# Optimization experiments

Measured on AMD Instinct MI355X. Metric: run time of the kernel, lower is better.

Reference implementation:

```python
import jax, jax.numpy as jnp
import numpy as np

IN_C = 256
OUT_C = 256
KQ_C = 256
HEADS = 8

def setup_inputs() -> dict:
    key = jax.random.key(0)
    kx, kq, kk, kv = jax.random.split(key, 4)
    N, T = 4, 2048
    x = jax.random.normal(kx, (N, IN_C, T), dtype=jnp.float32)
    # Conv1d(kernel_size=1, bias=False) weights: [out, in]
    s = 1.0 / np.sqrt(IN_C)
    Wq = jax.random.uniform(kq, (KQ_C, IN_C), dtype=jnp.float32, minval=-s, maxval=s)
    Wk = jax.random.uniform(kk, (KQ_C, IN_C), dtype=jnp.float32, minval=-s, maxval=s)
    Wv = jax.random.uniform(kv, (OUT_C, IN_C), dtype=jnp.float32, minval=-s, maxval=s)
    return {"x": x, "Wq": Wq, "Wk": Wk, "Wv": Wv}

def reference(x, Wq, Wk, Wv):
    N, C, T = x.shape
    H = HEADS
    dk = KQ_C // H   # head dim for q/k
    dv = OUT_C // H  # head dim for v
    # 1x1 conv == channel matmul: [N,C,T] -> [N,out,T]
    q = jnp.einsum('oc,nct->not', Wq, x).reshape(N, H, dk, T)
    k = jnp.einsum('oc,nct->not', Wk, x).reshape(N, H, dk, T)
    v = jnp.einsum('oc,nct->not', Wv, x).reshape(N, H, dv, T)
    # scores: [N,H,T,T] = q^T k, scaled
    scores = jnp.einsum('nhdt,nhds->nhts', q, k) / np.sqrt(dk).astype(jnp.float32)
    attn = jax.nn.softmax(scores, axis=-1)
    # out: [N,H,T,dv] -> [N,H,dv,T] -> [N,OUT_C,T]
    out = jnp.einsum('nhts,nhds->nhdt', attn, v)
    return out.reshape(N, OUT_C, T)
```

## Files before the change

kernel.cpp:

```cpp
#include <hip/hip_runtime.h>


typedef float f32x4 __attribute__((ext_vector_type(4)));
typedef short short8 __attribute__((ext_vector_type(8)));
typedef short short4v __attribute__((ext_vector_type(4)));

#define WS_Q 0u
#define WS_K (4u << 20)
#define WS_V (8u << 20)
#define WS_X (12u << 20)
#define WS_W (16u << 20)
#define WS_OP (20u << 20)

__device__ __forceinline__ unsigned short f2bf(float f) {
  unsigned int u = __builtin_bit_cast(unsigned int, f);
  u += 0x7FFFu + ((u >> 16) & 1u);
  return (unsigned short)(u >> 16);
}

__device__ __forceinline__ int pack_bf16rn(float a, float b) {
  unsigned int ua = __builtin_bit_cast(unsigned int, a) + 0x8000u;
  unsigned int ub = __builtin_bit_cast(unsigned int, b) + 0x8000u;
  return __builtin_amdgcn_perm(ub, ua, 0x07060302);
}

__global__ __launch_bounds__(256) void pack_kernel(
    const float* __restrict__ x, const float* __restrict__ Wq,
    const float* __restrict__ Wk, const float* __restrict__ Wv,
    unsigned short* __restrict__ ws) {
  const int tid = threadIdx.x;
  const int lane = tid & 63;
  const int wv = tid >> 6;
  const int lc = lane & 15, lq = lane >> 4;
  const int b = blockIdx.x;
  alignas(16) unsigned short tmp[8];
  if (b < 1024) {
    const int r = b * 4 + wv;
    const int kc = r & 7, tt = (r >> 3) & 127, n = r >> 10;
    const int t = tt * 16 + lc;
    const int c0 = kc * 32 + lq * 8;
    const float* src = x + (size_t)(n * 256 + c0) * 2048 + t;
#pragma unroll
    for (int j = 0; j < 8; ++j) tmp[j] = f2bf(src[(size_t)j * 2048]);
    unsigned short* dst = ws + (WS_X >> 1) + (size_t)r * 512 + lane * 8;
    *(int4*)dst = *(const int4*)tmp;
  } else {
    const int r = (b - 1024) * 4 + wv;
    const int kc = r & 7, ot = (r >> 3) & 15, wi = r >> 7;
    const float* W = (wi == 0) ? Wq : (wi == 1) ? Wk : Wv;
    const float scale = (wi == 0) ? 0.25503492f : 1.0f;
    const int o = ot * 16 + lc;
    const int c0 = kc * 32 + lq * 8;
    const float* src = W + o * 256 + c0;
#pragma unroll
    for (int j = 0; j < 8; ++j) tmp[j] = f2bf(src[j] * scale);
    unsigned short* dst = ws + (WS_W >> 1) + (size_t)r * 512 + lane * 8;
    *(int4*)dst = *(const int4*)tmp;
  }
}

__global__ __launch_bounds__(256) void proj_kernel(unsigned short* __restrict__ ws) {
  __shared__ unsigned short eps[4][2048];
  const int tid = threadIdx.x, lane = tid & 63, w = tid >> 6;
  const int lc = lane & 15, lq = lane >> 4;
  const int tt2 = blockIdx.x;
  const int n = blockIdx.y;
  const int wi = blockIdx.z;
  const unsigned short* Xb = ws + (WS_X >> 1);
  const unsigned short* Wb = ws + (WS_W >> 1);

  short8 af[2][8];
#pragma unroll
  for (int mt = 0; mt < 2; ++mt)
#pragma unroll
    for (int kc = 0; kc < 8; ++kc)
      af[mt][kc] = *(const short8*)(Xb + ((size_t)((n * 128 + tt2 * 2 + mt) * 8 + kc) * 512 + lane * 8));

  f32x4 acc[2][4];
#pragma unroll
  for (int mt = 0; mt < 2; ++mt)
#pragma unroll
    for (int nt = 0; nt < 4; ++nt) {
      f32x4 z = {0.f, 0.f, 0.f, 0.f};
      acc[mt][nt] = z;
    }

#pragma unroll
  for (int kc = 0; kc < 8; ++kc) {
    short8 bf[4];
#pragma unroll
    for (int nt = 0; nt < 4; ++nt)
      bf[nt] = *(const short8*)(Wb + ((size_t)((wi * 16 + w * 4 + nt) * 8 + kc) * 512 + lane * 8));
#pragma unroll
    for (int mt = 0; mt < 2; ++mt)
#pragma unroll
      for (int nt = 0; nt < 4; ++nt)
        acc[mt][nt] = __builtin_amdgcn_mfma_f32_16x16x32_bf16(af[mt][kc], bf[nt], acc[mt][nt], 0, 0, 0);
  }

  if (wi < 2) {
    unsigned short* ep = eps[w];
#pragma unroll
    for (int mt = 0; mt < 2; ++mt)
#pragma unroll
      for (int nt = 0; nt < 4; ++nt) {
        const int m2 = ((nt & 1) << 1) | (lc >> 3);
        const int base = ((mt * 2 + (nt >> 1)) << 9) + (m2 << 7) + (lq << 5) + (lc & 7);
#pragma unroll
        for (int r = 0; r < 4; ++r)
          ep[base + ((r ^ m2) << 3)] = f2bf(acc[mt][nt][r]);
      }
    const int swzl = lane ^ (lane >> 4);
    unsigned short* dst = ws + ((wi == 0) ? (WS_Q >> 1) : (WS_K >> 1));
#pragma unroll
    for (int rl = 0; rl < 4; ++rl) {
      int4 v = *(const int4*)(ep + (rl << 9) + swzl * 8);
      const int mt = rl >> 1, hh = rl & 1;
      const int nh = n * 8 + w * 2 + hh;
      const int ttg = tt2 * 2 + mt;
      *(int4*)(dst + ((size_t)(nh * 128 + ttg) * 64 + lane) * 8) = v;
    }
  } else {
    const int kb = tt2 >> 1, sbp = tt2 & 1;
#pragma unroll
    for (int nt = 0; nt < 4; ++nt) {
      const int nh = n * 8 + w * 2 + (nt >> 1);
      const int dt = nt & 1;
      alignas(16) unsigned short tmp[8];
#pragma unroll
      for (int mt = 0; mt < 2; ++mt)
#pragma unroll
        for (int r = 0; r < 4; ++r) tmp[mt * 4 + r] = f2bf(acc[mt][nt][r]);
      unsigned short* dstv = ws + (WS_V >> 1) +
          ((size_t)((((nh * 32 + kb) * 2 + dt) * 2 + sbp)) * 64 + lane) * 8;
      *(int4*)dstv = *(const int4*)tmp;
    }
  }
}

template <int KS>
__global__ __launch_bounds__(128, 5) void attn_kernel(
    const unsigned short* __restrict__ ws, float* __restrict__ out,
    unsigned short* __restrict__ opart, float* __restrict__ lpart) {
  const int tid = threadIdx.x;
  const int lane = tid & 63, wv = tid >> 6;
  const int lc = lane & 15, quad = lane >> 4;
  constexpr int CH = 32 * KS;
  const int c = blockIdx.x & (CH - 1);
  const int qx = blockIdx.x / CH;
  const int nh = c & 31;
  const int ks = c >> 5;
  const int qw = qx * 2 + wv;
  constexpr int NKB = 32 / KS;
  const int kb0 = ks * NKB;

  const unsigned short* Qw = ws + (WS_Q >> 1) + ((size_t)(nh * 128 + qw * 2)) * 512;
  const unsigned short* Kb = ws + (WS_K >> 1) + (size_t)nh * 65536;
  const unsigned short* Vb = ws + (WS_V >> 1) + (size_t)nh * 65536;

  short8 qf[2];
  qf[0] = *(const short8*)(Qw + lane * 8);
  qf[1] = *(const short8*)(Qw + 512 + lane * 8);

  f32x4 acc[2][2];
#pragma unroll
  for (int mt = 0; mt < 2; ++mt)
#pragma unroll
    for (int dt = 0; dt < 2; ++dt) {
      f32x4 z = {0.f, 0.f, 0.f, 0.f};
      acc[mt][dt] = z;
    }
  float lsum[2] = {0.f, 0.f};

  for (int kb = kb0; kb < kb0 + NKB; ++kb) {
    const unsigned short* kp = Kb + (size_t)kb * 2048 + lane * 8;
    const unsigned short* vp = Vb + (size_t)kb * 2048 + lane * 8;
    short8 kf[4], vvr[4];
#pragma unroll
    for (int sb = 0; sb < 4; ++sb) kf[sb] = *(const short8*)(kp + sb * 512);
#pragma unroll
    for (int u = 0; u < 4; ++u) vvr[u] = *(const short8*)(vp + u * 512);

    short4v pf[2][4];
#pragma unroll
    for (int mt = 0; mt < 2; ++mt) {
      f32x4 st[4];
#pragma unroll
      for (int sb = 0; sb < 4; ++sb) {
        f32x4 z = {0.f, 0.f, 0.f, 0.f};
        st[sb] = __builtin_amdgcn_mfma_f32_16x16x32_bf16(kf[sb], qf[mt], z, 0, 0, 0);
      }
#pragma unroll
      for (int sb = 0; sb < 4; ++sb) {
        float p0 = __builtin_amdgcn_exp2f(st[sb][0]);
        float p1 = __builtin_amdgcn_exp2f(st[sb][1]);
        float p2 = __builtin_amdgcn_exp2f(st[sb][2]);
        float p3 = __builtin_amdgcn_exp2f(st[sb][3]);
        lsum[mt] += (p0 + p1) + (p2 + p3);
        int2 pi;
        pi.x = pack_bf16rn(p0, p1);
        pi.y = pack_bf16rn(p2, p3);
        pf[mt][sb] = __builtin_bit_cast(short4v, pi);
      }
    }

    short4v vf[4][2];
#pragma unroll
    for (int dt = 0; dt < 2; ++dt)
#pragma unroll
      for (int sbp = 0; sbp < 2; ++sbp) {
        short8 t = vvr[dt * 2 + sbp];
        vf[sbp * 2 + 0][dt] = __builtin_shufflevector(t, t, 0, 1, 2, 3);
        vf[sbp * 2 + 1][dt] = __builtin_shufflevector(t, t, 4, 5, 6, 7);
      }
#pragma unroll
    for (int sb = 0; sb < 4; ++sb)
#pragma unroll
      for (int mt = 0; mt < 2; ++mt) {
        acc[mt][0] = __builtin_amdgcn_mfma_f32_16x16x16bf16_1k(pf[mt][sb], vf[sb][0], acc[mt][0], 0, 0, 0);
        acc[mt][1] = __builtin_amdgcn_mfma_f32_16x16x16bf16_1k(pf[mt][sb], vf[sb][1], acc[mt][1], 0, 0, 0);
      }
  }

#pragma unroll
  for (int mt = 0; mt < 2; ++mt) {
    lsum[mt] += __shfl_xor(lsum[mt], 16);
    lsum[mt] += __shfl_xor(lsum[mt], 32);
  }

  if constexpr (KS == 1) {
    const int chbase = (nh >> 3) * 256 + (nh & 7) * 32;
#pragma unroll
    for (int mt = 0; mt < 2; ++mt) {
      float is[4];
#pragma unroll
      for (int r = 0; r < 4; ++r) is[r] = 1.0f / __shfl(lsum[mt], quad * 4 + r);
      const int tb = qw * 32 + mt * 16 + quad * 4;
#pragma unroll
      for (int dt = 0; dt < 2; ++dt) {
        f32x4 ov;
#pragma unroll
        for (int r = 0; r < 4; ++r) ov[r] = acc[mt][dt][r] * is[r];
        *(f32x4*)(out + (size_t)(chbase + dt * 16 + lc) * 2048 + tb) = ov;
      }
    }
  } else {
    const size_t ob = (size_t)(ks * 32 + nh) * 32 * 2048;
#pragma unroll
    for (int mt = 0; mt < 2; ++mt) {
      const int tb = qw * 32 + mt * 16 + quad * 4;
#pragma unroll
      for (int dt = 0; dt < 2; ++dt) {
        int2 pi;
        pi.x = pack_bf16rn(acc[mt][dt][0], acc[mt][dt][1]);
        pi.y = pack_bf16rn(acc[mt][dt][2], acc[mt][dt][3]);
        *(int2*)(opart + ob + (size_t)(dt * 16 + lc) * 2048 + tb) = pi;
      }
      if (quad == 0)
        lpart[(size_t)(ks * 32 + nh) * 2048 + qw * 32 + mt * 16 + lc] = lsum[mt];
    }
  }
}

template <int KS>
__global__ __launch_bounds__(256) void finalize_kernel(
    const unsigned short* __restrict__ opart, const float* __restrict__ lpart,
    float* __restrict__ out) {
  const int f = blockIdx.x * 256 + threadIdx.x;
  const int t4 = f & 511;
  const int c = f >> 9;
  const int n = c >> 8, ch = c & 255;
  const int nh = n * 8 + (ch >> 5), d = ch & 31;
  float o[4] = {0.f, 0.f, 0.f, 0.f};
  float l[4] = {0.f, 0.f, 0.f, 0.f};
#pragma unroll
  for (int ks = 0; ks < KS; ++ks) {
    const short4v ov = *(const short4v*)(opart + ((size_t)(ks * 32 + nh) * 32 + d) * 2048 + t4 * 4);
    const float4 lv = *(const float4*)(lpart + (size_t)(ks * 32 + nh) * 2048 + t4 * 4);
#pragma unroll
    for (int i = 0; i < 4; ++i) {
      const unsigned int u = ((unsigned int)(unsigned short)ov[i]) << 16;
      o[i] += __builtin_bit_cast(float, u);
    }
    l[0] += lv.x; l[1] += lv.y; l[2] += lv.z; l[3] += lv.w;
  }
  float4 r;
  r.x = o[0] / l[0]; r.y = o[1] / l[1]; r.z = o[2] / l[2]; r.w = o[3] / l[3];
  *(float4*)(out + (size_t)f * 4) = r;
}

extern "C" void kernel_launch(void* const* d_in, const int* in_sizes, int n_in,
                              void* d_out, int out_size, void* d_ws, size_t ws_size,
                              hipStream_t stream) {
  const float* x = (const float*)d_in[0];
  const float* Wq = (const float*)d_in[1];
  const float* Wk = (const float*)d_in[2];
  const float* Wv = (const float*)d_in[3];
  unsigned short* ws = (unsigned short*)d_ws;
  float* out = (float*)d_out;
  (void)in_sizes; (void)n_in; (void)out_size;

  pack_kernel<<<1120, 256, 0, stream>>>(x, Wq, Wk, Wv, ws);
  proj_kernel<<<dim3(64, 4, 3), 256, 0, stream>>>(ws);

  char* wsb = (char*)d_ws;
  unsigned short* opart = (unsigned short*)(wsb + WS_OP);
  if (ws_size >= ((size_t)41u << 20)) {
    float* lpart = (float*)(wsb + WS_OP + ((size_t)4 * 4u << 20));
    attn_kernel<4><<<4096, 128, 0, stream>>>(ws, out, opart, lpart);
    finalize_kernel<4><<<2048, 256, 0, stream>>>(opart, lpart, out);
  } else if (ws_size >= ((size_t)30u << 20)) {
    float* lpart = (float*)(wsb + WS_OP + ((size_t)2 * 4u << 20));
    attn_kernel<2><<<2048, 128, 0, stream>>>(ws, out, opart, lpart);
    finalize_kernel<2><<<2048, 256, 0, stream>>>(opart, lpart, out);
  } else {
    attn_kernel<1><<<1024, 128, 0, stream>>>(ws, out, nullptr, nullptr);
  }
}
```

Measured before the change: 111.7 us.

## Double per-wave query tile to 64 rows to reuse K/V loads

Each wave now processes four 16-row query tiles instead of two, so every K and V fragment loaded from global memory is reused across twice as many queries. This halves the grid size and the total K/V traffic. The loop is reordered so QK MFMAs, exp and PV MFMAs are interleaved per key sub-block. The cost is higher register pressure, which is why the occupancy hint drops from 5 to 4 blocks per CU, and there are fewer blocks to fill the machine.

```diff
diff --git a/kernel.cpp b/kernel.cpp
--- a/kernel.cpp
+++ b/kernel.cpp
@@ -139,14 +139,14 @@
 }
 
 template <int KS>
-__global__ __launch_bounds__(128, 5) void attn_kernel(
+__global__ __launch_bounds__(128, 4) void attn_kernel(
     const unsigned short* __restrict__ ws, float* __restrict__ out,
     unsigned short* __restrict__ opart, float* __restrict__ lpart) {
   const int tid = threadIdx.x;
   const int lane = tid & 63, wv = tid >> 6;
   const int lc = lane & 15, quad = lane >> 4;
   constexpr int CH = 32 * KS;
-  const int c = blockIdx.x & (CH - 1);
+  const int c = blockIdx.x % CH;
   const int qx = blockIdx.x / CH;
   const int nh = c & 31;
   const int ks = c >> 5;
@@ -154,23 +154,23 @@
   constexpr int NKB = 32 / KS;
   const int kb0 = ks * NKB;
 
-  const unsigned short* Qw = ws + (WS_Q >> 1) + ((size_t)(nh * 128 + qw * 2)) * 512;
+  const unsigned short* Qw = ws + (WS_Q >> 1) + ((size_t)(nh * 128 + qw * 4)) * 512;
   const unsigned short* Kb = ws + (WS_K >> 1) + (size_t)nh * 65536;
   const unsigned short* Vb = ws + (WS_V >> 1) + (size_t)nh * 65536;
 
-  short8 qf[2];
-  qf[0] = *(const short8*)(Qw + lane * 8);
-  qf[1] = *(const short8*)(Qw + 512 + lane * 8);
-
-  f32x4 acc[2][2];
-#pragma unroll
-  for (int mt = 0; mt < 2; ++mt)
+  short8 qf[4];
+#pragma unroll
+  for (int mt = 0; mt < 4; ++mt) qf[mt] = *(const short8*)(Qw + mt * 512 + lane * 8);
+
+  f32x4 acc[4][2];
+#pragma unroll
+  for (int mt = 0; mt < 4; ++mt)
 #pragma unroll
     for (int dt = 0; dt < 2; ++dt) {
       f32x4 z = {0.f, 0.f, 0.f, 0.f};
       acc[mt][dt] = z;
     }
-  float lsum[2] = {0.f, 0.f};
+  float lsum[4] = {0.f, 0.f, 0.f, 0.f};
 
   for (int kb = kb0; kb < kb0 + NKB; ++kb) {
     const unsigned short* kp = Kb + (size_t)kb * 2048 + lane * 8;
@@ -181,49 +181,42 @@
 #pragma unroll
     for (int u = 0; u < 4; ++u) vvr[u] = *(const short8*)(vp + u * 512);
 
-    short4v pf[2][4];
-#pragma unroll
-    for (int mt = 0; mt < 2; ++mt) {
+#pragma unroll
+    for (int sb = 0; sb < 4; ++sb) {
       f32x4 st[4];
 #pragma unroll
-      for (int sb = 0; sb < 4; ++sb) {
+      for (int mt = 0; mt < 4; ++mt) {
         f32x4 z = {0.f, 0.f, 0.f, 0.f};
-        st[sb] = __builtin_amdgcn_mfma_f32_16x16x32_bf16(kf[sb], qf[mt], z, 0, 0, 0);
-      }
-#pragma unroll
-      for (int sb = 0; sb < 4; ++sb) {
-        float p0 = __builtin_amdgcn_exp2f(st[sb][0]);
-        float p1 = __builtin_amdgcn_exp2f(st[sb][1]);
-        float p2 = __builtin_amdgcn_exp2f(st[sb][2]);
-        float p3 = __builtin_amdgcn_exp2f(st[sb][3]);
+        st[mt] = __builtin_amdgcn_mfma_f32_16x16x32_bf16(kf[sb], qf[mt], z, 0, 0, 0);
+      }
+      short4v pfv[4];
+#pragma unroll
+      for (int mt = 0; mt < 4; ++mt) {
+        float p0 = __builtin_amdgcn_exp2f(st[mt][0]);
+        float p1 = __builtin_amdgcn_exp2f(st[mt][1]);
+        float p2 = __builtin_amdgcn_exp2f(st[mt][2]);
+        float p3 = __builtin_amdgcn_exp2f(st[mt][3]);
         lsum[mt] += (p0 + p1) + (p2 + p3);
         int2 pi;
         pi.x = pack_bf16rn(p0, p1);
         pi.y = pack_bf16rn(p2, p3);
-        pf[mt][sb] = __builtin_bit_cast(short4v, pi);
-      }
-    }
-
-    short4v vf[4][2];
-#pragma unroll
-    for (int dt = 0; dt < 2; ++dt)
-#pragma unroll
-      for (int sbp = 0; sbp < 2; ++sbp) {
-        short8 t = vvr[dt * 2 + sbp];
-        vf[sbp * 2 + 0][dt] = __builtin_shufflevector(t, t, 0, 1, 2, 3);
-        vf[sbp * 2 + 1][dt] = __builtin_shufflevector(t, t, 4, 5, 6, 7);
-      }
-#pragma unroll
-    for (int sb = 0; sb < 4; ++sb)
-#pragma unroll
-      for (int mt = 0; mt < 2; ++mt) {
-        acc[mt][0] = __builtin_amdgcn_mfma_f32_16x16x16bf16_1k(pf[mt][sb], vf[sb][0], acc[mt][0], 0, 0, 0);
-        acc[mt][1] = __builtin_amdgcn_mfma_f32_16x16x16bf16_1k(pf[mt][sb], vf[sb][1], acc[mt][1], 0, 0, 0);
-      }
-  }
-
-#pragma unroll
-  for (int mt = 0; mt < 2; ++mt) {
+        pfv[mt] = __builtin_bit_cast(short4v, pi);
+      }
+      const int sbp = sb >> 1, h = sb & 1;
+      short4v vf0 = h ? __builtin_shufflevector(vvr[sbp], vvr[sbp], 4, 5, 6, 7)
+                      : __builtin_shufflevector(vvr[sbp], vvr[sbp], 0, 1, 2, 3);
+      short4v vf1 = h ? __builtin_shufflevector(vvr[2 + sbp], vvr[2 + sbp], 4, 5, 6, 7)
+                      : __builtin_shufflevector(vvr[2 + sbp], vvr[2 + sbp], 0, 1, 2, 3);
+#pragma unroll
+      for (int mt = 0; mt < 4; ++mt) {
+        acc[mt][0] = __builtin_amdgcn_mfma_f32_16x16x16bf16_1k(pfv[mt], vf0, acc[mt][0], 0, 0, 0);
+        acc[mt][1] = __builtin_amdgcn_mfma_f32_16x16x16bf16_1k(pfv[mt], vf1, acc[mt][1], 0, 0, 0);
+      }
+    }
+  }
+
+#pragma unroll
+  for (int mt = 0; mt < 4; ++mt) {
     lsum[mt] += __shfl_xor(lsum[mt], 16);
     lsum[mt] += __shfl_xor(lsum[mt], 32);
   }
@@ -231,11 +224,11 @@
   if constexpr (KS == 1) {
     const int chbase = (nh >> 3) * 256 + (nh & 7) * 32;
 #pragma unroll
-    for (int mt = 0; mt < 2; ++mt) {
+    for (int mt = 0; mt < 4; ++mt) {
       float is[4];
 #pragma unroll
       for (int r = 0; r < 4; ++r) is[r] = 1.0f / __shfl(lsum[mt], quad * 4 + r);
-      const int tb = qw * 32 + mt * 16 + quad * 4;
+      const int tb = qw * 64 + mt * 16 + quad * 4;
 #pragma unroll
       for (int dt = 0; dt < 2; ++dt) {
         f32x4 ov;
@@ -247,8 +240,8 @@
   } else {
     const size_t ob = (size_t)(ks * 32 + nh) * 32 * 2048;
 #pragma unroll
-    for (int mt = 0; mt < 2; ++mt) {
-      const int tb = qw * 32 + mt * 16 + quad * 4;
+    for (int mt = 0; mt < 4; ++mt) {
+      const int tb = qw * 64 + mt * 16 + quad * 4;
 #pragma unroll
       for (int dt = 0; dt < 2; ++dt) {
         int2 pi;
@@ -257,7 +250,7 @@
         *(int2*)(opart + ob + (size_t)(dt * 16 + lc) * 2048 + tb) = pi;
       }
       if (quad == 0)
-        lpart[(size_t)(ks * 32 + nh) * 2048 + qw * 32 + mt * 16 + lc] = lsum[mt];
+        lpart[(size_t)(ks * 32 + nh) * 2048 + qw * 64 + mt * 16 + lc] = lsum[mt];
     }
   }
 }
@@ -307,13 +300,13 @@
   unsigned short* opart = (unsigned short*)(wsb + WS_OP);
   if (ws_size >= ((size_t)41u << 20)) {
     float* lpart = (float*)(wsb + WS_OP + ((size_t)4 * 4u << 20));
-    attn_kernel<4><<<4096, 128, 0, stream>>>(ws, out, opart, lpart);
+    attn_kernel<4><<<16 * 128, 128, 0, stream>>>(ws, out, opart, lpart);
     finalize_kernel<4><<<2048, 256, 0, stream>>>(opart, lpart, out);
   } else if (ws_size >= ((size_t)30u << 20)) {
     float* lpart = (float*)(wsb + WS_OP + ((size_t)2 * 4u << 20));
-    attn_kernel<2><<<2048, 128, 0, stream>>>(ws, out, opart, lpart);
+    attn_kernel<2><<<16 * 64, 128, 0, stream>>>(ws, out, opart, lpart);
     finalize_kernel<2><<<2048, 256, 0, stream>>>(opart, lpart, out);
   } else {
-    attn_kernel<1><<<1024, 128, 0, stream>>>(ws, out, nullptr, nullptr);
-  }
-}
+    attn_kernel<1><<<16 * 32, 128, 0, stream>>>(ws, out, nullptr, nullptr);
+  }
+}
```

Result: slower. 119.0 us (+6.5%).

## Fuse x bf16 packing into projection kernel and loop over Q/K/V weights

Applied to the files above, without the earlier changes.

The separate pass that converted x to bf16 fragments in workspace is removed. The projection kernel now loads a 256x32 fp32 tile of x into padded shared memory, converts it to bf16 MFMA fragments once, and reuses them across all three weight matrices in an in-kernel loop. This removes one intermediate write and read of x and a third of the projection blocks' redundant x loads. The cost is 34KB+ of LDS per block, fewer blocks (256 instead of 768), and a serial loop over Q/K/V inside each block.

```diff
diff --git a/kernel.cpp b/kernel.cpp
--- a/kernel.cpp
+++ b/kernel.cpp
@@ -8,7 +8,6 @@
 #define WS_Q 0u
 #define WS_K (4u << 20)
 #define WS_V (8u << 20)
-#define WS_X (12u << 20)
 #define WS_W (16u << 20)
 #define WS_OP (20u << 20)
 
@@ -24,116 +23,122 @@
   return __builtin_amdgcn_perm(ub, ua, 0x07060302);
 }
 
-__global__ __launch_bounds__(256) void pack_kernel(
-    const float* __restrict__ x, const float* __restrict__ Wq,
-    const float* __restrict__ Wk, const float* __restrict__ Wv,
-    unsigned short* __restrict__ ws) {
+__global__ __launch_bounds__(256) void pack_w_kernel(
+    const float* __restrict__ Wq, const float* __restrict__ Wk,
+    const float* __restrict__ Wv, unsigned short* __restrict__ ws) {
   const int tid = threadIdx.x;
   const int lane = tid & 63;
-  const int wv = tid >> 6;
   const int lc = lane & 15, lq = lane >> 4;
-  const int b = blockIdx.x;
+  const int r = blockIdx.x * 4 + (tid >> 6);
+  const int kc = r & 7, ot = (r >> 3) & 15, wi = r >> 7;
+  const float* W = (wi == 0) ? Wq : (wi == 1) ? Wk : Wv;
+  const float scale = (wi == 0) ? 0.25503492f : 1.0f;
+  const int o = ot * 16 + lc;
+  const int c0 = kc * 32 + lq * 8;
+  const float* src = W + o * 256 + c0;
   alignas(16) unsigned short tmp[8];
-  if (b < 1024) {
-    const int r = b * 4 + wv;
-    const int kc = r & 7, tt = (r >> 3) & 127, n = r >> 10;
-    const int t = tt * 16 + lc;
-    const int c0 = kc * 32 + lq * 8;
-    const float* src = x + (size_t)(n * 256 + c0) * 2048 + t;
-#pragma unroll
-    for (int j = 0; j < 8; ++j) tmp[j] = f2bf(src[(size_t)j * 2048]);
-    unsigned short* dst = ws + (WS_X >> 1) + (size_t)r * 512 + lane * 8;
-    *(int4*)dst = *(const int4*)tmp;
-  } else {
-    const int r = (b - 1024) * 4 + wv;
-    const int kc = r & 7, ot = (r >> 3) & 15, wi = r >> 7;
-    const float* W = (wi == 0) ? Wq : (wi == 1) ? Wk : Wv;
-    const float scale = (wi == 0) ? 0.25503492f : 1.0f;
-    const int o = ot * 16 + lc;
-    const int c0 = kc * 32 + lq * 8;
-    const float* src = W + o * 256 + c0;
-#pragma unroll
-    for (int j = 0; j < 8; ++j) tmp[j] = f2bf(src[j] * scale);
-    unsigned short* dst = ws + (WS_W >> 1) + (size_t)r * 512 + lane * 8;
-    *(int4*)dst = *(const int4*)tmp;
-  }
-}
-
-__global__ __launch_bounds__(256) void proj_kernel(unsigned short* __restrict__ ws) {
+#pragma unroll
+  for (int j = 0; j < 8; ++j) tmp[j] = f2bf(src[j] * scale);
+  unsigned short* dst = ws + (WS_W >> 1) + (size_t)r * 512 + lane * 8;
+  *(int4*)dst = *(const int4*)tmp;
+}
+
+__global__ __launch_bounds__(256) void proj_kernel(
+    const float* __restrict__ x, unsigned short* __restrict__ ws) {
+  __shared__ __align__(16) float xs[256 * 34];
   __shared__ unsigned short eps[4][2048];
   const int tid = threadIdx.x, lane = tid & 63, w = tid >> 6;
   const int lc = lane & 15, lq = lane >> 4;
   const int tt2 = blockIdx.x;
   const int n = blockIdx.y;
-  const int wi = blockIdx.z;
-  const unsigned short* Xb = ws + (WS_X >> 1);
+  const int tbase = tt2 * 32;
+
+  {
+    const float* xb = x + (size_t)n * 256 * 2048 + tbase;
+#pragma unroll
+    for (int k = 0; k < 8; ++k) {
+      const int i = tid + k * 256;
+      const int c = i >> 3, ch = i & 7;
+      float4 v = *(const float4*)(xb + (size_t)c * 2048 + ch * 4);
+      *(float4*)(xs + c * 34 + ch * 4) = v;
+    }
+  }
+  __syncthreads();
+
+  short8 af[2][8];
+#pragma unroll
+  for (int mt = 0; mt < 2; ++mt)
+#pragma unroll
+    for (int kc = 0; kc < 8; ++kc) {
+      alignas(16) unsigned short t8[8];
+#pragma unroll
+      for (int j = 0; j < 8; ++j)
+        t8[j] = f2bf(xs[(kc * 32 + lq * 8 + j) * 34 + mt * 16 + lc]);
+      af[mt][kc] = *(const short8*)t8;
+    }
+
   const unsigned short* Wb = ws + (WS_W >> 1);
 
-  short8 af[2][8];
-#pragma unroll
-  for (int mt = 0; mt < 2; ++mt)
-#pragma unroll
-    for (int kc = 0; kc < 8; ++kc)
-      af[mt][kc] = *(const short8*)(Xb + ((size_t)((n * 128 + tt2 * 2 + mt) * 8 + kc) * 512 + lane * 8));
-
-  f32x4 acc[2][4];
-#pragma unroll
-  for (int mt = 0; mt < 2; ++mt)
-#pragma unroll
-    for (int nt = 0; nt < 4; ++nt) {
-      f32x4 z = {0.f, 0.f, 0.f, 0.f};
-      acc[mt][nt] = z;
-    }
-
-#pragma unroll
-  for (int kc = 0; kc < 8; ++kc) {
-    short8 bf[4];
-#pragma unroll
-    for (int nt = 0; nt < 4; ++nt)
-      bf[nt] = *(const short8*)(Wb + ((size_t)((wi * 16 + w * 4 + nt) * 8 + kc) * 512 + lane * 8));
+  for (int wi = 0; wi < 3; ++wi) {
+    f32x4 acc[2][4];
 #pragma unroll
     for (int mt = 0; mt < 2; ++mt)
 #pragma unroll
+      for (int nt = 0; nt < 4; ++nt) {
+        f32x4 z = {0.f, 0.f, 0.f, 0.f};
+        acc[mt][nt] = z;
+      }
+
+#pragma unroll
+    for (int kc = 0; kc < 8; ++kc) {
+      short8 bf[4];
+#pragma unroll
       for (int nt = 0; nt < 4; ++nt)
-        acc[mt][nt] = __builtin_amdgcn_mfma_f32_16x16x32_bf16(af[mt][kc], bf[nt], acc[mt][nt], 0, 0, 0);
-  }
-
-  if (wi < 2) {
-    unsigned short* ep = eps[w];
-#pragma unroll
-    for (int mt = 0; mt < 2; ++mt)
+        bf[nt] = *(const short8*)(Wb + ((size_t)((wi * 16 + w * 4 + nt) * 8 + kc) * 512 + lane * 8));
+#pragma unroll
+      for (int mt = 0; mt < 2; ++mt)
+#pragma unroll
+        for (int nt = 0; nt < 4; ++nt)
+          acc[mt][nt] = __builtin_amdgcn_mfma_f32_16x16x32_bf16(af[mt][kc], bf[nt], acc[mt][nt], 0, 0, 0);
+    }
+
+    if (wi < 2) {
+      unsigned short* ep = eps[w];
+#pragma unroll
+      for (int mt = 0; mt < 2; ++mt)
+#pragma unroll
+        for (int nt = 0; nt < 4; ++nt) {
+          const int m2 = ((nt & 1) << 1) | (lc >> 3);
+          const int base = ((mt * 2 + (nt >> 1)) << 9) + (m2 << 7) + (lq << 5) + (lc & 7);
+#pragma unroll
+          for (int r = 0; r < 4; ++r)
+            ep[base + ((r ^ m2) << 3)] = f2bf(acc[mt][nt][r]);
+        }
+      const int swzl = lane ^ (lane >> 4);
+      unsigned short* dst = ws + ((wi == 0) ? (WS_Q >> 1) : (WS_K >> 1));
+#pragma unroll
+      for (int rl = 0; rl < 4; ++rl) {
+        int4 v = *(const int4*)(ep + (rl << 9) + swzl * 8);
+        const int mt = rl >> 1, hh = rl & 1;
+        const int nh = n * 8 + w * 2 + hh;
+        const int ttg = tt2 * 2 + mt;
+        *(int4*)(dst + ((size_t)(nh * 128 + ttg) * 64 + lane) * 8) = v;
+      }
+    } else {
+      const int kb = tt2 >> 1, sbp = tt2 & 1;
 #pragma unroll
       for (int nt = 0; nt < 4; ++nt) {
-        const int m2 = ((nt & 1) << 1) | (lc >> 3);
-        const int base = ((mt * 2 + (nt >> 1)) << 9) + (m2 << 7) + (lq << 5) + (lc & 7);
-#pragma unroll
-        for (int r = 0; r < 4; ++r)
-          ep[base + ((r ^ m2) << 3)] = f2bf(acc[mt][nt][r]);
-      }
-    const int swzl = lane ^ (lane >> 4);
-    unsigned short* dst = ws + ((wi == 0) ? (WS_Q >> 1) : (WS_K >> 1));
-#pragma unroll
-    for (int rl = 0; rl < 4; ++rl) {
-      int4 v = *(const int4*)(ep + (rl << 9) + swzl * 8);
-      const int mt = rl >> 1, hh = rl & 1;
-      const int nh = n * 8 + w * 2 + hh;
-      const int ttg = tt2 * 2 + mt;
-      *(int4*)(dst + ((size_t)(nh * 128 + ttg) * 64 + lane) * 8) = v;
-    }
-  } else {
-    const int kb = tt2 >> 1, sbp = tt2 & 1;
-#pragma unroll
-    for (int nt = 0; nt < 4; ++nt) {
-      const int nh = n * 8 + w * 2 + (nt >> 1);
-      const int dt = nt & 1;
-      alignas(16) unsigned short tmp[8];
-#pragma unroll
-      for (int mt = 0; mt < 2; ++mt)
-#pragma unroll
-        for (int r = 0; r < 4; ++r) tmp[mt * 4 + r] = f2bf(acc[mt][nt][r]);
-      unsigned short* dstv = ws + (WS_V >> 1) +
-          ((size_t)((((nh * 32 + kb) * 2 + dt) * 2 + sbp)) * 64 + lane) * 8;
-      *(int4*)dstv = *(const int4*)tmp;
+        const int nh = n * 8 + w * 2 + (nt >> 1);
+        const int dt = nt & 1;
+        alignas(16) unsigned short tmp[8];
+#pragma unroll
+        for (int mt = 0; mt < 2; ++mt)
+#pragma unroll
+          for (int r = 0; r < 4; ++r) tmp[mt * 4 + r] = f2bf(acc[mt][nt][r]);
+        unsigned short* dstv = ws + (WS_V >> 1) +
+            ((size_t)((((nh * 32 + kb) * 2 + dt) * 2 + sbp)) * 64 + lane) * 8;
+        *(int4*)dstv = *(const int4*)tmp;
+      }
     }
   }
 }
@@ -300,8 +305,8 @@
   float* out = (float*)d_out;
   (void)in_sizes; (void)n_in; (void)out_size;
 
-  pack_kernel<<<1120, 256, 0, stream>>>(x, Wq, Wk, Wv, ws);
-  proj_kernel<<<dim3(64, 4, 3), 256, 0, stream>>>(ws);
+  pack_w_kernel<<<96, 256, 0, stream>>>(Wq, Wk, Wv, ws);
+  proj_kernel<<<dim3(64, 4), 256, 0, stream>>>(x, ws);
 
   char* wsb = (char*)d_ws;
   unsigned short* opart = (unsigned short*)(wsb + WS_OP);
```

Measured after the change: 119.3 us. 6.8% more time.
